# Optimization experiments

Hardware: AMD Instinct MI355X
Metric: run time of the kernel (lower is better)

Reference implementation:

```python
import jax, jax.numpy as jnp
import numpy as np

C = 256  # in_channels
B, N = 8, 2048


def setup_inputs() -> dict:
    key = jax.random.key(0)
    ks = jax.random.split(key, 9)
    s = 1.0 / np.sqrt(C)  # conv1d default init scale (approx)
    return {
        "x": jax.random.normal(ks[0], (B, C, N), jnp.float32),
        "wq": jax.random.normal(ks[1], (C, C), jnp.float32) * s,
        "bq": jax.random.normal(ks[2], (C,), jnp.float32) * s,
        "wk": jax.random.normal(ks[3], (C, C), jnp.float32) * s,
        "bk": jax.random.normal(ks[4], (C,), jnp.float32) * s,
        "wv": jax.random.normal(ks[5], (C, C), jnp.float32) * s,
        "bv": jax.random.normal(ks[6], (C,), jnp.float32) * s,
        "wo": jax.random.normal(ks[7], (C, C), jnp.float32) * s,
        "bo": jax.random.normal(ks[8], (C,), jnp.float32) * s,
    }


def reference(x, wq, bq, wk, bk, wv, bv, wo, bo):
    # 1x1 Conv1d == channel-wise linear: [C_out,C_in] x [B,C_in,N] -> [B,C_out,N]
    proj = lambda w, b, t: jnp.einsum('ci,bin->bcn', w, t) + b[None, :, None]
    q = proj(wq, bq, x)
    k = proj(wk, bk, x)
    v = proj(wv, bv, x)
    norm = 1.0 / (x.shape[1] ** 0.5)
    # scores: w[b,n,m] = sum_c q[b,c,n] k[b,c,m]
    w = jnp.einsum('bcn,bcm->bnm', q, k) * norm
    w = jax.nn.softmax(w, axis=2)
    # attn output: sum_m v[b,c,m] w[b,n,m] -> [B,C,N]
    av = jnp.einsum('bcm,bnm->bcn', v, w)
    out = proj(wo, bo, av)
    return x + out
```

## Files before the change

kernel.cpp:

```cpp
#include <hip/hip_runtime.h>
#include <hip/hip_bf16.h>

#define CCH 256
#define NSEQ 2048
#define BATCH 8

typedef __hip_bfloat16 bf16;
typedef short s8v __attribute__((ext_vector_type(8)));
typedef float f4v __attribute__((ext_vector_type(4)));
typedef float f16v __attribute__((ext_vector_type(16)));

struct __align__(8) bf16x4 { bf16 v[4]; };

__device__ __forceinline__ float b2f(bf16 h) { return __bfloat162float(h); }
__device__ __forceinline__ bf16 f2b(float f) { return __float2bfloat16(f); }

#define MFMA16(a, b, c) __builtin_amdgcn_mfma_f32_16x16x32_bf16((a), (b), (c), 0, 0, 0)
#define MFMA32(a, b, c) __builtin_amdgcn_mfma_f32_32x32x16_bf16((a), (b), (c), 0, 0, 0)

__device__ __forceinline__ void gload_lds16(const bf16* g, bf16* l) {
    __builtin_amdgcn_global_load_lds(
        (const __attribute__((address_space(1))) unsigned int*)(g),
        (__attribute__((address_space(3))) unsigned int*)(l), 16, 0, 0);
}

__global__ __launch_bounds__(256) void prepw_kernel(
    const float* __restrict__ wq, const float* __restrict__ wk,
    const float* __restrict__ wv, const float* __restrict__ wo,
    bf16* __restrict__ wqb, bf16* __restrict__ wkb,
    bf16* __restrict__ wvb, bf16* __restrict__ wob)
{
    int base = (blockIdx.x * 256 + threadIdx.x) * 8;
    int mat = base >> 16, off = base & 65535;
    const float* s = (mat == 0) ? wq : (mat == 1) ? wk : (mat == 2) ? wv : wo;
    bf16* d = (mat == 0) ? wqb : (mat == 1) ? wkb : (mat == 2) ? wvb : wob;
    int doff = (mat == 3) ? off : (off ^ (((off >> 8) & 7) << 3));
    bf16 tmp[8];
    #pragma unroll
    for (int j = 0; j < 8; ++j) tmp[j] = f2b(s[off + j]);
    *(s8v*)&d[doff] = *(const s8v*)tmp;
}

__global__ __launch_bounds__(512, 4) void qkvprep_kernel(
    const float* __restrict__ x,
    const bf16* __restrict__ Wq, const bf16* __restrict__ Wk,
    const bf16* __restrict__ Wv,
    const float* __restrict__ bq, const float* __restrict__ bk,
    const float* __restrict__ bv,
    bf16* __restrict__ qTt, bf16* __restrict__ kTt, bf16* __restrict__ Vt)
{
    __shared__ bf16 xs[64][260];
    __shared__ bf16 wbuf[2][2][4096];

    const int tile = blockIdx.x;
    const int flat0 = tile * 64;
    const int phase = blockIdx.y;
    const int b = flat0 >> 11, nn = flat0 & 2047;
    const int tid = threadIdx.x;
    const int w = tid >> 6, lane = tid & 63;
    const int l15 = lane & 15, quad = lane >> 4;
    const int ng = w & 3;
    const int ch = w >> 2;
    const float* xb = x + (size_t)b * CCH * NSEQ;

    bf16* qt = qTt + (size_t)tile * 16384;
    bf16* kt = kTt + (size_t)tile * 16384;
    bf16* Vtb = Vt + (size_t)b * CCH * NSEQ;

    auto chunk_ptr = [&](int j) -> const bf16* {
        if (phase == 0)
            return (j < 8) ? Wq + (size_t)(ch * 8 + j) * 4096
                           : Wk + (size_t)(ch * 4 + (j - 8)) * 4096;
        else
            return (j < 8) ? Wv + (size_t)(ch * 8 + j) * 4096
                           : Wk + (size_t)(8 + ch * 4 + (j - 8)) * 4096;
    };
    auto stage = [&](int j, int par) {
        const bf16* src = chunk_ptr(j);
        bf16* dst = &wbuf[ch][par][0];
        int seg = (w & 3) * 2;
        gload_lds16(src + (seg + 0) * 512 + lane * 8, dst + (seg + 0) * 512);
        gload_lds16(src + (seg + 1) * 512 + lane * 8, dst + (seg + 1) * 512);
    };

    stage(0, 0);
    #pragma unroll
    for (int i = 0; i < 8; ++i) {
        int f4i = i * 512 + tid;
        int c = f4i >> 4, nq = f4i & 15;
        float4 v4 = *(const float4*)&xb[(size_t)c * NSEQ + nn + nq * 4];
        xs[nq * 4 + 0][c] = f2b(v4.x);
        xs[nq * 4 + 1][c] = f2b(v4.y);
        xs[nq * 4 + 2][c] = f2b(v4.z);
        xs[nq * 4 + 3][c] = f2b(v4.w);
    }
    __syncthreads();

    s8v xf[8];
    #pragma unroll
    for (int t = 0; t < 8; ++t)
        xf[t] = *(const s8v*)&xs[ng * 16 + l15][t * 32 + quad * 8];

    int par = 0;
    #pragma unroll
    for (int j = 0; j < 12; ++j) {
        if (j < 11) stage(j + 1, par ^ 1);

        const char* wb = (const char*)&wbuf[ch][par][0];
        s8v wf[8];
        #pragma unroll
        for (int t = 0; t < 8; ++t)
            wf[t] = *(const s8v*)(wb + l15 * 512 +
                                  ((t * 64 + quad * 16) ^ ((l15 & 7) << 4)));

        if (phase == 0 || j >= 8) {
            f4v a0 = {}, a1 = {};
            #pragma unroll
            for (int t = 0; t < 4; ++t) {
                a0 = MFMA16(wf[t], xf[t], a0);
                a1 = MFMA16(wf[t + 4], xf[t + 4], a1);
            }
            const bool isq = (phase == 0) && (j < 8);
            const int cs = (phase == 0)
                ? (j < 8 ? ch * 8 + j : ch * 4 + (j - 8))
                : (8 + ch * 4 + (j - 8));
            const float* bm = isq ? bq : bk;
            bf16* ot = isq ? qt : kt;
            const float sc = isq ? 0.0625f : 1.0f;
            float4 bb4 = *(const float4*)&bm[cs * 16 + quad * 4];
            float bbr[4] = { bb4.x, bb4.y, bb4.z, bb4.w };
            bf16x4 pk;
            #pragma unroll
            for (int r = 0; r < 4; ++r)
                pk.v[r] = f2b((a0[r] + a1[r] + bbr[r]) * sc);
            int nl = ng * 16 + l15;
            *(bf16x4*)&ot[(cs * 2 + (quad >> 1)) * 512 + nl * 8 + (quad & 1) * 4] = pk;
        } else {
            f4v a0 = {}, a1 = {};
            #pragma unroll
            for (int t = 0; t < 4; ++t) {
                a0 = MFMA16(xf[t], wf[t], a0);
                a1 = MFMA16(xf[t + 4], wf[t + 4], a1);
            }
            const int cs = ch * 8 + j;
            int c = cs * 16 + l15;
            float bb = bv[c];
            bf16x4 pk;
            #pragma unroll
            for (int r = 0; r < 4; ++r)
                pk.v[r] = f2b(a0[r] + a1[r] + bb);
            const int m16 = (nn >> 4) + ng;
            size_t e0 = ((size_t)m16 * 256 + c) * 16 + (quad >> 1) * 8 + (quad & 1) * 4;
            *(bf16x4*)&Vtb[e0] = pk;
        }
        __syncthreads();
        par ^= 1;
    }
}

__global__ __launch_bounds__(256, 2) void flash_kernel(
    const bf16* __restrict__ qTt, const bf16* __restrict__ kTt,
    const bf16* __restrict__ Vt, bf16* __restrict__ Opart,
    float* __restrict__ lpart)
{
    __shared__ bf16 Kc[16384];
    __shared__ bf16 Ps[64][68];
    __shared__ float l_s[2][64];

    const int b = blockIdx.x, nt = blockIdx.y, ms = blockIdx.z;
    const int tid = threadIdx.x;
    const int W = tid >> 6, lane = tid & 63;
    const int l31 = lane & 31, h = lane >> 5;
    const int ng = W >> 1, mg = W & 1;
    const int mb = ms * 16;
    const bf16* Vtb = Vt + (size_t)b * CCH * NSEQ;

    s8v qf[16];
    {
        const bf16* qt = qTt + (size_t)(b * 32 + nt) * 16384;
        #pragma unroll
        for (int t = 0; t < 16; ++t)
            qf[t] = *(const s8v*)&qt[(t * 2 + h) * 512 + (ng * 32 + l31) * 8];
    }
    const bf16* vbase = Vtb + (size_t)(W * 64 + l31) * 16 + h * 8;

    f16v O[2][2] = {};
    float lsum = 0.f;

    auto stageK = [&](int a) {
        const bf16* kt = kTt + (size_t)(b * 32 + a) * 16384;
        #pragma unroll
        for (int i = 0; i < 8; ++i) {
            int ch = W * 8 + i;
            gload_lds16(kt + ch * 512 + lane * 8, &Kc[ch * 512]);
        }
    };

    stageK(mb);
    __syncthreads();

    for (int mt = 0; mt < 16; ++mt) {
        f16v S0 = {}, S1 = {};
        __builtin_amdgcn_s_setprio(1);
        #pragma unroll
        for (int t = 0; t < 8; ++t) {
            s8v kf0 = *(const s8v*)&Kc[(t * 2 + h) * 512 + (mg * 32 + l31) * 8];
            s8v kf1 = *(const s8v*)&Kc[((t + 8) * 2 + h) * 512 + (mg * 32 + l31) * 8];
            S0 = MFMA32(kf0, qf[t], S0);
            S1 = MFMA32(kf1, qf[t + 8], S1);
        }
        __builtin_amdgcn_s_setprio(0);
        s8v vf[2][4];
        #pragma unroll
        for (int ks = 0; ks < 4; ++ks)
            #pragma unroll
            for (int cr = 0; cr < 2; ++cr)
                vf[cr][ks] = *(const s8v*)(vbase
                    + (size_t)((mb + mt) * 4 + ks) * 4096 + cr * 512);
        #pragma unroll
        for (int q = 0; q < 4; ++q) {
            bf16x4 pk;
            #pragma unroll
            for (int r = 0; r < 4; ++r) {
                float e = __expf(fminf(S0[q * 4 + r] + S1[q * 4 + r], 60.f));
                lsum += e;
                pk.v[r] = f2b(e);
            }
            *(bf16x4*)&Ps[ng * 32 + l31][mg * 32 + q * 8 + h * 4] = pk;
        }
        __syncthreads();

        if (mt < 15) stageK(mb + mt + 1);

        __builtin_amdgcn_s_setprio(1);
        #pragma unroll
        for (int ks = 0; ks < 4; ++ks) {
            s8v pf0 = *(const s8v*)&Ps[l31][ks * 16 + h * 8];
            s8v pf1 = *(const s8v*)&Ps[32 + l31][ks * 16 + h * 8];
            O[0][0] = MFMA32(vf[0][ks], pf0, O[0][0]);
            O[0][1] = MFMA32(vf[0][ks], pf1, O[0][1]);
            O[1][0] = MFMA32(vf[1][ks], pf0, O[1][0]);
            O[1][1] = MFMA32(vf[1][ks], pf1, O[1][1]);
        }
        __builtin_amdgcn_s_setprio(0);
        __syncthreads();
    }

    {
        float s = lsum + __shfl_xor(lsum, 32);
        if (h == 0) l_s[mg][ng * 32 + l31] = s;
    }
    __syncthreads();
    const size_t pb = (size_t)(b * 32 + nt) * 2 + ms;
    if (tid < 64) lpart[pb * 64 + tid] = l_s[0][tid] + l_s[1][tid];

    bf16* Ob = Opart + pb * 16384;
    #pragma unroll
    for (int cr = 0; cr < 2; ++cr)
        #pragma unroll
        for (int g2 = 0; g2 < 2; ++g2) {
            int n = g2 * 32 + l31;
            #pragma unroll
            for (int q2 = 0; q2 < 4; ++q2) {
                bf16x4 pk;
                #pragma unroll
                for (int j = 0; j < 4; ++j) pk.v[j] = f2b(O[cr][g2][q2 * 4 + j]);
                int c = W * 64 + cr * 32 + q2 * 8 + 4 * h;
                *(bf16x4*)&Ob[(size_t)n * 256 + c] = pk;
            }
        }
}

__global__ __launch_bounds__(512, 4) void outproj_kernel(
    const bf16* __restrict__ Opart, const float* __restrict__ lpart,
    const bf16* __restrict__ Wob, const float* __restrict__ bo,
    const float* __restrict__ x, float* __restrict__ out)
{
    __shared__ bf16 avs[64][260];
    __shared__ float ils[64];

    const int bx = blockIdx.x;
    const int flat0 = bx * 64;
    const int c0 = blockIdx.y * 128;
    const int tid = threadIdx.x;
    const int w = tid >> 6, lane = tid & 63;
    const int l15 = lane & 15, quad = lane >> 4;

    if (tid < 64)
        ils[tid] = 1.f / (lpart[(size_t)(bx * 2) * 64 + tid]
                        + lpart[(size_t)(bx * 2 + 1) * 64 + tid]);
    __syncthreads();

    const bf16x4* O0 = (const bf16x4*)(Opart + (size_t)(bx * 2) * 16384);
    const bf16x4* O1 = O0 + 4096;
    #pragma unroll
    for (int i = 0; i < 8; ++i) {
        int u = i * 512 + tid;
        int n = u >> 6;
        bf16x4 a = O0[u], bb = O1[u];
        float il = ils[n];
        bf16x4 o;
        #pragma unroll
        for (int t = 0; t < 4; ++t)
            o.v[t] = f2b((b2f(a.v[t]) + b2f(bb.v[t])) * il);
        *(bf16x4*)&avs[n][(u & 63) * 4] = o;
    }
    __syncthreads();

    const int bidx = flat0 >> 11, nn = flat0 & 2047;
    const size_t base = (size_t)bidx * CCH * NSEQ;
    const int cg = c0 + w * 16;

    s8v af[8];
    #pragma unroll
    for (int t = 0; t < 8; ++t)
        af[t] = *(const s8v*)&Wob[(size_t)(cg + l15) * CCH + t * 32 + quad * 8];

    f4v O[4] = {};
    #pragma unroll
    for (int nt = 0; nt < 4; ++nt)
        #pragma unroll
        for (int t = 0; t < 8; ++t) {
            s8v br = *(const s8v*)&avs[nt * 16 + l15][t * 32 + quad * 8];
            O[nt] = MFMA16(af[t], br, O[nt]);
        }
    #pragma unroll
    for (int r = 0; r < 4; ++r) {
        int c = cg + quad * 4 + r;
        float bb = bo[c];
        #pragma unroll
        for (int nt = 0; nt < 4; ++nt) {
            size_t idx = base + (size_t)c * NSEQ + nn + nt * 16 + l15;
            out[idx] = O[nt][r] + bb + x[idx];
        }
    }
}

extern "C" void kernel_launch(void* const* d_in, const int* in_sizes, int n_in,
                              void* d_out, int out_size, void* d_ws, size_t ws_size,
                              hipStream_t stream) {
    (void)in_sizes; (void)n_in; (void)out_size; (void)ws_size;
    const float* x  = (const float*)d_in[0];
    const float* wq = (const float*)d_in[1];
    const float* bq = (const float*)d_in[2];
    const float* wk = (const float*)d_in[3];
    const float* bk = (const float*)d_in[4];
    const float* wv = (const float*)d_in[5];
    const float* bv = (const float*)d_in[6];
    const float* wo = (const float*)d_in[7];
    const float* bo = (const float*)d_in[8];
    float* out = (float*)d_out;

    const size_t T = (size_t)BATCH * CCH * NSEQ;
    bf16* qTt  = (bf16*)d_ws;
    bf16* kTt  = qTt + T;
    bf16* Vt   = kTt + T;
    bf16* wqb  = Vt + T;
    bf16* wkb  = wqb + 65536;
    bf16* wvb  = wkb + 65536;
    bf16* wob  = wvb + 65536;
    float* lpart = (float*)(wob + 65536);
    bf16* Opart  = (bf16*)(lpart + 32768);

    prepw_kernel<<<128, 256, 0, stream>>>(wq, wk, wv, wo, wqb, wkb, wvb, wob);
    qkvprep_kernel<<<dim3(256, 2), 512, 0, stream>>>(
        x, wqb, wkb, wvb, bq, bk, bv, qTt, kTt, Vt);
    flash_kernel<<<dim3(8, 32, 2), 256, 0, stream>>>(qTt, kTt, Vt, Opart, lpart);
    outproj_kernel<<<dim3(256, 2), 512, 0, stream>>>(Opart, lpart, wob, bo, x, out);
}
```

Measured before the change: 155.0 us.

## Process two K tiles per loop iteration to halve barrier count

The flash loop now stages two K tiles and two P tiles in double-sized LDS buffers and computes scores for both before one barrier, then runs the PV MFMAs for both. This halves the number of __syncthreads per block and gives more independent MFMA work between barriers. In exchange LDS use roughly doubles (about 82KB per block with launch bounds 2) and register pressure rises from holding twice the V fragments, which may reduce occupancy or cause spills.

```diff
diff --git a/kernel.cpp b/kernel.cpp
--- a/kernel.cpp
+++ b/kernel.cpp
@@ -163,8 +163,8 @@
     const bf16* __restrict__ Vt, bf16* __restrict__ Opart,
     float* __restrict__ lpart)
 {
-    __shared__ bf16 Kc[16384];
-    __shared__ bf16 Ps[64][68];
+    __shared__ bf16 Kc[2][16384];
+    __shared__ bf16 Ps[2][64][68];
     __shared__ float l_s[2][64];
 
     const int b = blockIdx.x, nt = blockIdx.y, ms = blockIdx.z;
@@ -187,61 +187,70 @@
     f16v O[2][2] = {};
     float lsum = 0.f;
 
-    auto stageK = [&](int a) {
+    auto stageK = [&](int a, int buf) {
         const bf16* kt = kTt + (size_t)(b * 32 + a) * 16384;
         #pragma unroll
         for (int i = 0; i < 8; ++i) {
             int ch = W * 8 + i;
-            gload_lds16(kt + ch * 512 + lane * 8, &Kc[ch * 512]);
+            gload_lds16(kt + ch * 512 + lane * 8, &Kc[buf][ch * 512]);
         }
     };
 
-    stageK(mb);
-    __syncthreads();
-
-    for (int mt = 0; mt < 16; ++mt) {
-        f16v S0 = {}, S1 = {};
+    stageK(mb + 0, 0);
+    stageK(mb + 1, 1);
+    __syncthreads();
+
+    for (int t8 = 0; t8 < 8; ++t8) {
+        s8v vf[2][2][4];
+        #pragma unroll
+        for (int u = 0; u < 2; ++u) {
+            const int mt = mb + t8 * 2 + u;
+            f16v S0 = {}, S1 = {};
+            __builtin_amdgcn_s_setprio(1);
+            #pragma unroll
+            for (int t = 0; t < 8; ++t) {
+                s8v kf0 = *(const s8v*)&Kc[u][(t * 2 + h) * 512 + (mg * 32 + l31) * 8];
+                s8v kf1 = *(const s8v*)&Kc[u][((t + 8) * 2 + h) * 512 + (mg * 32 + l31) * 8];
+                S0 = MFMA32(kf0, qf[t], S0);
+                S1 = MFMA32(kf1, qf[t + 8], S1);
+            }
+            __builtin_amdgcn_s_setprio(0);
+            #pragma unroll
+            for (int ks = 0; ks < 4; ++ks)
+                #pragma unroll
+                for (int cr = 0; cr < 2; ++cr)
+                    vf[u][cr][ks] = *(const s8v*)(vbase
+                        + (size_t)(mt * 4 + ks) * 4096 + cr * 512);
+            #pragma unroll
+            for (int q = 0; q < 4; ++q) {
+                bf16x4 pk;
+                #pragma unroll
+                for (int r = 0; r < 4; ++r) {
+                    float e = __expf(fminf(S0[q * 4 + r] + S1[q * 4 + r], 60.f));
+                    lsum += e;
+                    pk.v[r] = f2b(e);
+                }
+                *(bf16x4*)&Ps[u][ng * 32 + l31][mg * 32 + q * 8 + h * 4] = pk;
+            }
+        }
+        __syncthreads();
+
+        if (t8 < 7) {
+            stageK(mb + t8 * 2 + 2, 0);
+            stageK(mb + t8 * 2 + 3, 1);
+        }
         __builtin_amdgcn_s_setprio(1);
         #pragma unroll
-        for (int t = 0; t < 8; ++t) {
-            s8v kf0 = *(const s8v*)&Kc[(t * 2 + h) * 512 + (mg * 32 + l31) * 8];
-            s8v kf1 = *(const s8v*)&Kc[((t + 8) * 2 + h) * 512 + (mg * 32 + l31) * 8];
-            S0 = MFMA32(kf0, qf[t], S0);
-            S1 = MFMA32(kf1, qf[t + 8], S1);
-        }
-        __builtin_amdgcn_s_setprio(0);
-        s8v vf[2][4];
-        #pragma unroll
-        for (int ks = 0; ks < 4; ++ks)
-            #pragma unroll
-            for (int cr = 0; cr < 2; ++cr)
-                vf[cr][ks] = *(const s8v*)(vbase
-                    + (size_t)((mb + mt) * 4 + ks) * 4096 + cr * 512);
-        #pragma unroll
-        for (int q = 0; q < 4; ++q) {
-            bf16x4 pk;
-            #pragma unroll
-            for (int r = 0; r < 4; ++r) {
-                float e = __expf(fminf(S0[q * 4 + r] + S1[q * 4 + r], 60.f));
-                lsum += e;
-                pk.v[r] = f2b(e);
-            }
-            *(bf16x4*)&Ps[ng * 32 + l31][mg * 32 + q * 8 + h * 4] = pk;
-        }
-        __syncthreads();
-
-        if (mt < 15) stageK(mb + mt + 1);
-
-        __builtin_amdgcn_s_setprio(1);
-        #pragma unroll
-        for (int ks = 0; ks < 4; ++ks) {
-            s8v pf0 = *(const s8v*)&Ps[l31][ks * 16 + h * 8];
-            s8v pf1 = *(const s8v*)&Ps[32 + l31][ks * 16 + h * 8];
-            O[0][0] = MFMA32(vf[0][ks], pf0, O[0][0]);
-            O[0][1] = MFMA32(vf[0][ks], pf1, O[0][1]);
-            O[1][0] = MFMA32(vf[1][ks], pf0, O[1][0]);
-            O[1][1] = MFMA32(vf[1][ks], pf1, O[1][1]);
-        }
+        for (int u = 0; u < 2; ++u)
+            #pragma unroll
+            for (int ks = 0; ks < 4; ++ks) {
+                s8v pf0 = *(const s8v*)&Ps[u][l31][ks * 16 + h * 8];
+                s8v pf1 = *(const s8v*)&Ps[u][32 + l31][ks * 16 + h * 8];
+                O[0][0] = MFMA32(vf[u][0][ks], pf0, O[0][0]);
+                O[0][1] = MFMA32(vf[u][0][ks], pf1, O[0][1]);
+                O[1][0] = MFMA32(vf[u][1][ks], pf0, O[1][0]);
+                O[1][1] = MFMA32(vf[u][1][ks], pf1, O[1][1]);
+            }
         __builtin_amdgcn_s_setprio(0);
         __syncthreads();
     }
```

Measured after the change: 167.8 us. +8.2%, slower.
